# Kernel tuning notes

Hardware: AMD Instinct MI355X
Metric: run time of the kernel (lower is better)

## Reference

```python
import jax, jax.numpy as jnp
import numpy as np

TIME_STEP = 0.02  # matches init_kwargs
B, T, D = 128, 2048, 4


def setup_inputs() -> dict:
    key = jax.random.key(0)
    k1, k2, k3, k4 = jax.random.split(key, 4)
    return {
        "h_real": jax.random.normal(k1, (B, T, D, D), dtype=jnp.float32),
        "h_imag": jax.random.normal(k2, (B, T, D, D), dtype=jnp.float32),
        "s_real": jax.random.normal(k3, (B, D, D), dtype=jnp.float32),
        "s_imag": jax.random.normal(k4, (B, D, D), dtype=jnp.float32),
    }


def reference(h_real, h_imag, s_real, s_imag):
    # dt = -1j * time_step (complex64 scalar, as in the keras cell)
    dt = jnp.asarray(-1j * TIME_STEP, dtype=jnp.complex64)
    H = (h_real + 1j * h_imag).astype(jnp.complex64)        # [B,T,D,D]
    state0 = (s_real + 1j * s_imag).astype(jnp.complex64)    # [B,D,D]
    Hs = jnp.transpose(H, (1, 0, 2, 3))                       # [T,B,D,D] for scan

    def step(state, h_t):
        # unitary = expm(-i*dt*H_t), batched over B via expm's leading-dim batching
        unitary = jax.scipy.linalg.expm(h_t * dt)             # [B,D,D]
        new_state = jnp.matmul(unitary, state)                # [B,D,D]
        return new_state, new_state

    _, seq = jax.lax.scan(step, state0, Hs)                   # seq: [T,B,D,D] complex64
    # return real/imag stacked so downstream harness sees a real tensor
    return jnp.stack([seq.real, seq.imag])                    # [2,T,B,D,D] float32
```

## Files before the change

### kernel.cpp

```cpp
#include <hip/hip_runtime.h>

namespace {

constexpr int    TT     = 2048;
constexpr int    BB     = 128;
constexpr int    CHUNK  = 8;
constexpr int    NCHUNK = TT / CHUNK;
constexpr float  DT     = 0.02f;
constexpr size_t HALF   = (size_t)TT * BB * 16;

__device__ __forceinline__ void cmm(const float* __restrict__ ar, const float* __restrict__ ai,
                                    const float* __restrict__ br, const float* __restrict__ bi,
                                    float* __restrict__ cr, float* __restrict__ ci) {
#pragma unroll
    for (int i = 0; i < 4; ++i) {
#pragma unroll
        for (int j = 0; j < 4; ++j) {
            float sr = 0.f, si = 0.f;
#pragma unroll
            for (int k = 0; k < 4; ++k) {
                const float xr = ar[i * 4 + k], xi = ai[i * 4 + k];
                const float yr = br[k * 4 + j], yi = bi[k * 4 + j];
                sr = fmaf(xr, yr, sr);
                sr = fmaf(-xi, yi, sr);
                si = fmaf(xr, yi, si);
                si = fmaf(xi, yr, si);
            }
            cr[i * 4 + j] = sr;
            ci[i * 4 + j] = si;
        }
    }
}

__device__ __forceinline__ unsigned int pack2(float a, float b) {
    return (__float_as_uint(a) >> 16) | (__float_as_uint(b) & 0xFFFF0000u);
}
__device__ __forceinline__ float unlo(unsigned int u) { return __uint_as_float(u << 16); }
__device__ __forceinline__ float unhi(unsigned int u) { return __uint_as_float(u & 0xFFFF0000u); }

}

__global__ __launch_bounds__(256) void kA_expm_scan(const float* __restrict__ hr,
                                                    const float* __restrict__ hi,
                                                    uint4* __restrict__ L,
                                                    float* __restrict__ totals) {
    const int gid  = blockIdx.x * 256 + threadIdx.x;
    const int b    = gid >> 11;
    const int t    = gid & (TT - 1);
    const int sub  = t & (CHUNK - 1);
    const int c    = t >> 3;
    const int lane = threadIdx.x & 63;

    float a_r[16], a_i[16];
    {
        const float4* p4r = reinterpret_cast<const float4*>(hr) + (size_t)gid * 4;
        const float4* p4i = reinterpret_cast<const float4*>(hi) + (size_t)gid * 4;
#pragma unroll
        for (int v = 0; v < 4; ++v) {
            const float4 rr = p4r[v];
            const float4 im = p4i[v];
            a_r[v * 4 + 0] = DT * im.x;  a_i[v * 4 + 0] = -DT * rr.x;
            a_r[v * 4 + 1] = DT * im.y;  a_i[v * 4 + 1] = -DT * rr.y;
            a_r[v * 4 + 2] = DT * im.z;  a_i[v * 4 + 2] = -DT * rr.z;
            a_r[v * 4 + 3] = DT * im.w;  a_i[v * 4 + 3] = -DT * rr.w;
        }
    }

    float er[16], ei[16];
    {
        float a2r[16], a2i[16];
        cmm(a_r, a_i, a_r, a_i, a2r, a2i);
        float tr[16], ti[16];
#pragma unroll
        for (int e = 0; e < 16; ++e) {
            const float d = (e % 5 == 0) ? 1.0f : 0.0f;
            tr[e] = fmaf(a_r[e], 1.f / 6.f, d * 0.5f);
            tr[e] = fmaf(a2r[e], 1.f / 24.f, tr[e]);
            ti[e] = a_i[e] * (1.f / 6.f);
            ti[e] = fmaf(a2i[e], 1.f / 24.f, ti[e]);
        }
        cmm(a2r, a2i, tr, ti, er, ei);
#pragma unroll
        for (int e = 0; e < 16; ++e) {
            const float d = (e % 5 == 0) ? 1.0f : 0.0f;
            er[e] = er[e] + d + a_r[e];
            ei[e] = ei[e] + a_i[e];
        }
    }

#pragma unroll
    for (int d = 1; d < CHUNK; d <<= 1) {
        int src = lane - d;
        if (src < 0) src = 0;
        float qr[16], qi[16];
#pragma unroll
        for (int e = 0; e < 16; ++e) {
            qr[e] = __shfl(er[e], src, 64);
            qi[e] = __shfl(ei[e], src, 64);
        }
        float nr[16], ni[16];
        cmm(er, ei, qr, qi, nr, ni);
        const bool pred = (sub >= d);
#pragma unroll
        for (int e = 0; e < 16; ++e) {
            er[e] = pred ? nr[e] : er[e];
            ei[e] = pred ? ni[e] : ei[e];
        }
    }

    if (sub == CHUNK - 1) {
        float* tp = totals + ((size_t)b * NCHUNK + c) * 32;
#pragma unroll
        for (int e = 0; e < 16; ++e) {
            tp[e]      = er[e];
            tp[16 + e] = ei[e];
        }
    }

    {
        uint4 w0, w1, w2, w3;
        w0.x = pack2(er[0],  er[1]);   w0.y = pack2(er[2],  er[3]);
        w0.z = pack2(er[4],  er[5]);   w0.w = pack2(er[6],  er[7]);
        w1.x = pack2(er[8],  er[9]);   w1.y = pack2(er[10], er[11]);
        w1.z = pack2(er[12], er[13]);  w1.w = pack2(er[14], er[15]);
        w2.x = pack2(ei[0],  ei[1]);   w2.y = pack2(ei[2],  ei[3]);
        w2.z = pack2(ei[4],  ei[5]);   w2.w = pack2(ei[6],  ei[7]);
        w3.x = pack2(ei[8],  ei[9]);   w3.y = pack2(ei[10], ei[11]);
        w3.z = pack2(ei[12], ei[13]);  w3.w = pack2(ei[14], ei[15]);
        uint4* Lp = L + (size_t)gid * 4;
        Lp[0] = w0; Lp[1] = w1; Lp[2] = w2; Lp[3] = w3;
    }
}

__global__ __launch_bounds__(256) void kC_carry(const float* __restrict__ totals,
                                                const float* __restrict__ sr,
                                                const float* __restrict__ si,
                                                float* __restrict__ carry) {
    __shared__ float sRe[16][NCHUNK];
    __shared__ float sIm[16][NCHUNK];

    const int ct = threadIdx.x;
    const int b  = blockIdx.x;

    float pr[16], pi[16];
    if (ct == 0) {
#pragma unroll
        for (int e = 0; e < 16; ++e) {
            pr[e] = sr[b * 16 + e];
            pi[e] = si[b * 16 + e];
        }
    } else {
        const float* tp = totals + ((size_t)b * NCHUNK + ct - 1) * 32;
#pragma unroll
        for (int e = 0; e < 16; ++e) {
            pr[e] = tp[e];
            pi[e] = tp[16 + e];
        }
    }

#pragma unroll
    for (int e = 0; e < 16; ++e) {
        sRe[e][ct] = pr[e];
        sIm[e][ct] = pi[e];
    }
    __syncthreads();

#pragma unroll
    for (int d = 1; d < NCHUNK; d <<= 1) {
        if (ct >= d) {
            float qr[16], qi[16];
#pragma unroll
            for (int e = 0; e < 16; ++e) {
                qr[e] = sRe[e][ct - d];
                qi[e] = sIm[e][ct - d];
            }
            float nr[16], ni[16];
            cmm(pr, pi, qr, qi, nr, ni);
#pragma unroll
            for (int e = 0; e < 16; ++e) {
                pr[e] = nr[e];
                pi[e] = ni[e];
            }
        }
        __syncthreads();
        if (ct >= d) {
#pragma unroll
            for (int e = 0; e < 16; ++e) {
                sRe[e][ct] = pr[e];
                sIm[e][ct] = pi[e];
            }
        }
        __syncthreads();
    }

    float* cp = carry + ((size_t)b * NCHUNK + ct) * 32;
#pragma unroll
    for (int e = 0; e < 16; ++e) {
        cp[e]      = pr[e];
        cp[16 + e] = pi[e];
    }
}

__global__ __launch_bounds__(256) void kD_final(const uint4* __restrict__ L,
                                                const float* __restrict__ carry,
                                                float* __restrict__ out) {
    __shared__ float lds[32 * 16 * 17];

    const int bid   = blockIdx.x;
    const int tileT = bid & 127;
    const int tileB = bid >> 7;
    const int t0 = tileT * 16, b0 = tileB * 16;
    const int tid = threadIdx.x;

    {
        const int bloc = tid >> 4, tloc = tid & 15;
        const int tt = t0 + tloc;
        const size_t gi = ((size_t)(b0 + bloc) * TT + tt);

        const uint4* Lp = L + gi * 4;
        const uint4 w0 = Lp[0], w1 = Lp[1], w2 = Lp[2], w3 = Lp[3];
        float l_r[16], l_i[16];
        l_r[0]  = unlo(w0.x); l_r[1]  = unhi(w0.x); l_r[2]  = unlo(w0.y); l_r[3]  = unhi(w0.y);
        l_r[4]  = unlo(w0.z); l_r[5]  = unhi(w0.z); l_r[6]  = unlo(w0.w); l_r[7]  = unhi(w0.w);
        l_r[8]  = unlo(w1.x); l_r[9]  = unhi(w1.x); l_r[10] = unlo(w1.y); l_r[11] = unhi(w1.y);
        l_r[12] = unlo(w1.z); l_r[13] = unhi(w1.z); l_r[14] = unlo(w1.w); l_r[15] = unhi(w1.w);
        l_i[0]  = unlo(w2.x); l_i[1]  = unhi(w2.x); l_i[2]  = unlo(w2.y); l_i[3]  = unhi(w2.y);
        l_i[4]  = unlo(w2.z); l_i[5]  = unhi(w2.z); l_i[6]  = unlo(w2.w); l_i[7]  = unhi(w2.w);
        l_i[8]  = unlo(w3.x); l_i[9]  = unhi(w3.x); l_i[10] = unlo(w3.y); l_i[11] = unhi(w3.y);
        l_i[12] = unlo(w3.z); l_i[13] = unhi(w3.z); l_i[14] = unlo(w3.w); l_i[15] = unhi(w3.w);

        float c_r[16], c_i[16];
        const float* cp = carry + ((size_t)(b0 + bloc) * NCHUNK + (tt >> 3)) * 32;
#pragma unroll
        for (int e = 0; e < 16; ++e) {
            c_r[e] = cp[e];
            c_i[e] = cp[16 + e];
        }

        float o_r[16], o_i[16];
        cmm(l_r, l_i, c_r, c_i, o_r, o_i);

        const int slot = bloc * 17 + tloc;
#pragma unroll
        for (int e = 0; e < 16; ++e) {
            lds[e * 272 + slot]        = o_r[e];
            lds[(e + 16) * 272 + slot] = o_i[e];
        }
    }
    __syncthreads();

    {
        const int u = tid >> 4;
        const int v = tid & 15;
        const int slot = v * 17 + u;

        float r2[16], i2[16];
#pragma unroll
        for (int e = 0; e < 16; ++e) {
            r2[e] = lds[e * 272 + slot];
            i2[e] = lds[(e + 16) * 272 + slot];
        }

        const size_t oi = ((size_t)(t0 + u) * BB + (b0 + v)) * 16;
        float4* orp = reinterpret_cast<float4*>(out + oi);
        float4* oip = reinterpret_cast<float4*>(out + HALF + oi);
#pragma unroll
        for (int w = 0; w < 4; ++w) {
            orp[w] = make_float4(r2[w * 4 + 0], r2[w * 4 + 1], r2[w * 4 + 2], r2[w * 4 + 3]);
            oip[w] = make_float4(i2[w * 4 + 0], i2[w * 4 + 1], i2[w * 4 + 2], i2[w * 4 + 3]);
        }
    }
}

extern "C" void kernel_launch(void* const* d_in, const int* in_sizes, int n_in,
                              void* d_out, int out_size, void* d_ws, size_t ws_size,
                              hipStream_t stream) {
    const float* hr = (const float*)d_in[0];
    const float* hi = (const float*)d_in[1];
    const float* sr = (const float*)d_in[2];
    const float* si = (const float*)d_in[3];
    float* out    = (float*)d_out;
    float* totals = (float*)d_ws;
    float* carry  = (float*)d_ws + (size_t)BB * NCHUNK * 32;
    uint4* L      = (uint4*)((float*)d_ws + 2 * (size_t)BB * NCHUNK * 32);

    kA_expm_scan<<<(BB * TT) / 256, 256, 0, stream>>>(hr, hi, L, totals);
    kC_carry    <<<BB, 256, 0, stream>>>(totals, sr, si, carry);
    kD_final    <<<(BB * TT) / 256, 256, 0, stream>>>(L, carry, out);
}
```

Before: 121.6 us.

## Use fp16 for intermediate L, nontemporal loads/stores, and swizzle final block order

Switches the packed intermediate chunk-local products from truncated bf16 to round-to-nearest fp16, which keeps more mantissa precision at the same storage size. Marks the input H loads and the output stores as nontemporal to reduce cache pollution on single-use streams. Remaps block indices in the final kernel so consecutive blocks touch different time tiles, changing the DRAM and L2 access pattern. fp16 has a narrower range than bf16, so large unitary-product entries could overflow, although the values here should be bounded.

```diff
diff --git a/kernel.cpp b/kernel.cpp
--- a/kernel.cpp
+++ b/kernel.cpp
@@ -1,4 +1,6 @@
 #include <hip/hip_runtime.h>
+#include <hip/hip_fp16.h>
+#include <cstring>
 
 namespace {
 
@@ -8,6 +10,8 @@
 constexpr int    NCHUNK = TT / CHUNK;
 constexpr float  DT     = 0.02f;
 constexpr size_t HALF   = (size_t)TT * BB * 16;
+
+typedef float vf4 __attribute__((ext_vector_type(4)));
 
 __device__ __forceinline__ void cmm(const float* __restrict__ ar, const float* __restrict__ ai,
                                     const float* __restrict__ br, const float* __restrict__ bi,
@@ -32,11 +36,17 @@
     }
 }
 
-__device__ __forceinline__ unsigned int pack2(float a, float b) {
-    return (__float_as_uint(a) >> 16) | (__float_as_uint(b) & 0xFFFF0000u);
-}
-__device__ __forceinline__ float unlo(unsigned int u) { return __uint_as_float(u << 16); }
-__device__ __forceinline__ float unhi(unsigned int u) { return __uint_as_float(u & 0xFFFF0000u); }
+__device__ __forceinline__ unsigned int pkh(float a, float b) {
+    __half2 h = __floats2half2_rn(a, b);
+    unsigned int u;
+    __builtin_memcpy(&u, &h, 4);
+    return u;
+}
+__device__ __forceinline__ float2 uph(unsigned int u) {
+    __half2 h;
+    __builtin_memcpy(&h, &u, 4);
+    return __half22float2(h);
+}
 
 }
 
@@ -53,16 +63,17 @@
 
     float a_r[16], a_i[16];
     {
-        const float4* p4r = reinterpret_cast<const float4*>(hr) + (size_t)gid * 4;
-        const float4* p4i = reinterpret_cast<const float4*>(hi) + (size_t)gid * 4;
+        const vf4* p4r = reinterpret_cast<const vf4*>(hr) + (size_t)gid * 4;
+        const vf4* p4i = reinterpret_cast<const vf4*>(hi) + (size_t)gid * 4;
 #pragma unroll
         for (int v = 0; v < 4; ++v) {
-            const float4 rr = p4r[v];
-            const float4 im = p4i[v];
-            a_r[v * 4 + 0] = DT * im.x;  a_i[v * 4 + 0] = -DT * rr.x;
-            a_r[v * 4 + 1] = DT * im.y;  a_i[v * 4 + 1] = -DT * rr.y;
-            a_r[v * 4 + 2] = DT * im.z;  a_i[v * 4 + 2] = -DT * rr.z;
-            a_r[v * 4 + 3] = DT * im.w;  a_i[v * 4 + 3] = -DT * rr.w;
+            const vf4 rr = __builtin_nontemporal_load(p4r + v);
+            const vf4 im = __builtin_nontemporal_load(p4i + v);
+#pragma unroll
+            for (int e = 0; e < 4; ++e) {
+                a_r[v * 4 + e] = DT * im[e];
+                a_i[v * 4 + e] = -DT * rr[e];
+            }
         }
     }
 
@@ -119,14 +130,14 @@
 
     {
         uint4 w0, w1, w2, w3;
-        w0.x = pack2(er[0],  er[1]);   w0.y = pack2(er[2],  er[3]);
-        w0.z = pack2(er[4],  er[5]);   w0.w = pack2(er[6],  er[7]);
-        w1.x = pack2(er[8],  er[9]);   w1.y = pack2(er[10], er[11]);
-        w1.z = pack2(er[12], er[13]);  w1.w = pack2(er[14], er[15]);
-        w2.x = pack2(ei[0],  ei[1]);   w2.y = pack2(ei[2],  ei[3]);
-        w2.z = pack2(ei[4],  ei[5]);   w2.w = pack2(ei[6],  ei[7]);
-        w3.x = pack2(ei[8],  ei[9]);   w3.y = pack2(ei[10], ei[11]);
-        w3.z = pack2(ei[12], ei[13]);  w3.w = pack2(ei[14], ei[15]);
+        w0.x = pkh(er[0],  er[1]);   w0.y = pkh(er[2],  er[3]);
+        w0.z = pkh(er[4],  er[5]);   w0.w = pkh(er[6],  er[7]);
+        w1.x = pkh(er[8],  er[9]);   w1.y = pkh(er[10], er[11]);
+        w1.z = pkh(er[12], er[13]);  w1.w = pkh(er[14], er[15]);
+        w2.x = pkh(ei[0],  ei[1]);   w2.y = pkh(ei[2],  ei[3]);
+        w2.z = pkh(ei[4],  ei[5]);   w2.w = pkh(ei[6],  ei[7]);
+        w3.x = pkh(ei[8],  ei[9]);   w3.y = pkh(ei[10], ei[11]);
+        w3.z = pkh(ei[12], ei[13]);  w3.w = pkh(ei[14], ei[15]);
         uint4* Lp = L + (size_t)gid * 4;
         Lp[0] = w0; Lp[1] = w1; Lp[2] = w2; Lp[3] = w3;
     }
@@ -206,9 +217,9 @@
                                                 float* __restrict__ out) {
     __shared__ float lds[32 * 16 * 17];
 
-    const int bid   = blockIdx.x;
-    const int tileT = bid & 127;
-    const int tileB = bid >> 7;
+    const int g     = blockIdx.x;
+    const int tileT = (g & 7) * 16 + ((g >> 3) & 15);
+    const int tileB = g >> 7;
     const int t0 = tileT * 16, b0 = tileB * 16;
     const int tid = threadIdx.x;
 
@@ -220,14 +231,25 @@
         const uint4* Lp = L + gi * 4;
         const uint4 w0 = Lp[0], w1 = Lp[1], w2 = Lp[2], w3 = Lp[3];
         float l_r[16], l_i[16];
-        l_r[0]  = unlo(w0.x); l_r[1]  = unhi(w0.x); l_r[2]  = unlo(w0.y); l_r[3]  = unhi(w0.y);
-        l_r[4]  = unlo(w0.z); l_r[5]  = unhi(w0.z); l_r[6]  = unlo(w0.w); l_r[7]  = unhi(w0.w);
-        l_r[8]  = unlo(w1.x); l_r[9]  = unhi(w1.x); l_r[10] = unlo(w1.y); l_r[11] = unhi(w1.y);
-        l_r[12] = unlo(w1.z); l_r[13] = unhi(w1.z); l_r[14] = unlo(w1.w); l_r[15] = unhi(w1.w);
-        l_i[0]  = unlo(w2.x); l_i[1]  = unhi(w2.x); l_i[2]  = unlo(w2.y); l_i[3]  = unhi(w2.y);
-        l_i[4]  = unlo(w2.z); l_i[5]  = unhi(w2.z); l_i[6]  = unlo(w2.w); l_i[7]  = unhi(w2.w);
-        l_i[8]  = unlo(w3.x); l_i[9]  = unhi(w3.x); l_i[10] = unlo(w3.y); l_i[11] = unhi(w3.y);
-        l_i[12] = unlo(w3.z); l_i[13] = unhi(w3.z); l_i[14] = unlo(w3.w); l_i[15] = unhi(w3.w);
+        {
+            float2 p;
+            p = uph(w0.x); l_r[0]  = p.x; l_r[1]  = p.y;
+            p = uph(w0.y); l_r[2]  = p.x; l_r[3]  = p.y;
+            p = uph(w0.z); l_r[4]  = p.x; l_r[5]  = p.y;
+            p = uph(w0.w); l_r[6]  = p.x; l_r[7]  = p.y;
+            p = uph(w1.x); l_r[8]  = p.x; l_r[9]  = p.y;
+            p = uph(w1.y); l_r[10] = p.x; l_r[11] = p.y;
+            p = uph(w1.z); l_r[12] = p.x; l_r[13] = p.y;
+            p = uph(w1.w); l_r[14] = p.x; l_r[15] = p.y;
+            p = uph(w2.x); l_i[0]  = p.x; l_i[1]  = p.y;
+            p = uph(w2.y); l_i[2]  = p.x; l_i[3]  = p.y;
+            p = uph(w2.z); l_i[4]  = p.x; l_i[5]  = p.y;
+            p = uph(w2.w); l_i[6]  = p.x; l_i[7]  = p.y;
+            p = uph(w3.x); l_i[8]  = p.x; l_i[9]  = p.y;
+            p = uph(w3.y); l_i[10] = p.x; l_i[11] = p.y;
+            p = uph(w3.z); l_i[12] = p.x; l_i[13] = p.y;
+            p = uph(w3.w); l_i[14] = p.x; l_i[15] = p.y;
+        }
 
         float c_r[16], c_i[16];
         const float* cp = carry + ((size_t)(b0 + bloc) * NCHUNK + (tt >> 3)) * 32;
@@ -262,12 +284,14 @@
         }
 
         const size_t oi = ((size_t)(t0 + u) * BB + (b0 + v)) * 16;
-        float4* orp = reinterpret_cast<float4*>(out + oi);
-        float4* oip = reinterpret_cast<float4*>(out + HALF + oi);
+        vf4* orp = reinterpret_cast<vf4*>(out + oi);
+        vf4* oip = reinterpret_cast<vf4*>(out + HALF + oi);
 #pragma unroll
         for (int w = 0; w < 4; ++w) {
-            orp[w] = make_float4(r2[w * 4 + 0], r2[w * 4 + 1], r2[w * 4 + 2], r2[w * 4 + 3]);
-            oip[w] = make_float4(i2[w * 4 + 0], i2[w * 4 + 1], i2[w * 4 + 2], i2[w * 4 + 3]);
+            vf4 vr = {r2[w * 4 + 0], r2[w * 4 + 1], r2[w * 4 + 2], r2[w * 4 + 3]};
+            vf4 vi = {i2[w * 4 + 0], i2[w * 4 + 1], i2[w * 4 + 2], i2[w * 4 + 3]};
+            __builtin_nontemporal_store(vr, orp + w);
+            __builtin_nontemporal_store(vi, oip + w);
         }
     }
 }
```

Result: slower. 161.4 us (+32.8%).
